# Optimization experiments

Measured on AMD Instinct MI355X. Metric: run time of the kernel, lower is better.

The kernel has to match this reference:

```python
import jax, jax.numpy as jnp
import numpy as np
from jax import lax

L, CB, D, K = 4, 256, 512, 3   # layers, bottleneck, dconv_size, kernel
B, T = 16, 4096                # batch, frames
EPS = 1e-5


def _binarize(w):
    # bitwise weight quantization: sign(w), straight-through in bwd
    return w + lax.stop_gradient(jnp.sign(w) - w)


def _conv1d(x, w, b, dilation=1, groups=1, pad=(0, 0)):
    # x: [N, C, T], w: [O, I/groups, K]
    y = lax.conv_general_dilated(
        x, w, window_strides=(1,), padding=[pad], rhs_dilation=(dilation,),
        dimension_numbers=("NCH", "OIH", "NCH"), feature_group_count=groups)
    return y + b[None, :, None]


def _prelu(x, a):
    return jnp.where(x >= 0, x, a * x)


def _bn(x, g, b):
    # training-mode BatchNorm1d over (batch, time) per channel
    mean = jnp.mean(x, axis=(0, 2), keepdims=True)
    var = jnp.var(x, axis=(0, 2), keepdims=True)
    xn = (x - mean) * lax.rsqrt(var + EPS)
    return xn * g[None, :, None] + b[None, :, None]


def setup_inputs() -> dict:
    key = jax.random.key(0)
    ks = jax.random.split(key, 8)
    s = 0.05
    return {
        "x":   jax.random.normal(ks[0], (B, CB, T), jnp.float32),
        "w1":  jax.random.normal(ks[1], (L, D, CB, 1), jnp.float32) * s,
        "b1":  jnp.zeros((L, D), jnp.float32),
        "a1":  jnp.full((L,), 0.25, jnp.float32),
        "g1":  jnp.ones((L, D), jnp.float32),
        "be1": jnp.zeros((L, D), jnp.float32),
        "wd":  jax.random.normal(ks[2], (L, D, 1, K), jnp.float32) * s,
        "bd":  jnp.zeros((L, D), jnp.float32),
        "a2":  jnp.full((L,), 0.25, jnp.float32),
        "g2":  jnp.ones((L, D), jnp.float32),
        "be2": jnp.zeros((L, D), jnp.float32),
        "w2":  jax.random.normal(ks[3], (L, CB, D, 1), jnp.float32) * s,
        "b2":  jnp.zeros((L, CB), jnp.float32),
    }


def reference(x, w1, b1, a1, g1, be1, wd, bd, a2, g2, be2, w2, b2):
    resid = x
    for i in range(L):
        dil = 2 ** i
        pad_left = dil * (K - 1)  # causal/chomped padding keeps length T
        x = _conv1d(x, _binarize(w1[i]), b1[i])                       # 1x1: CB->D
        x = _bn(_prelu(x, a1[i]), g1[i], be1[i])
        x = _conv1d(x, _binarize(wd[i]), bd[i], dilation=dil,
                    groups=D, pad=(pad_left, 0))                       # depthwise dilated
        x = _bn(_prelu(x, a2[i]), g2[i], be2[i])
        x = _conv1d(x, _binarize(w2[i]), b2[i])                       # 1x1: D->CB
    return x + resid
```

## Files before the change

kernel.cpp:

```cpp
#include <hip/hip_runtime.h>
#include <stdint.h>
#include <stddef.h>

#define NL   4
#define CBC  256
#define DCH  512
#define KW   3
#define BATCH 16
#define TT   4096
#define BT   (BATCH*TT)
#define EPSB 1e-5f

typedef __bf16 bf16_t;
typedef __attribute__((ext_vector_type(8))) __bf16 bf16x8;
typedef __attribute__((ext_vector_type(4))) float f32x4;
typedef __attribute__((ext_vector_type(8))) unsigned short us8;
typedef __attribute__((ext_vector_type(4))) unsigned short us4;

static __device__ __forceinline__ unsigned short f2bf(float f) {
    union { float f; uint32_t u; } v; v.f = f;
    uint32_t u = v.u;
    u += 0x7FFFu + ((u >> 16) & 1u);
    return (unsigned short)(u >> 16);
}
static __device__ __forceinline__ float bf2f(unsigned short b) {
    union { uint32_t u; float f; } v; v.u = ((uint32_t)b) << 16;
    return v.f;
}
static __device__ __forceinline__ bf16x8 as_bf16x8(us8 u) {
    return __builtin_bit_cast(bf16x8, u);
}
static __device__ __forceinline__ float signf_(float w) {
    return (w > 0.f) ? 1.f : ((w < 0.f) ? -1.f : 0.f);
}

typedef __attribute__((address_space(1))) void as1_void;
typedef __attribute__((address_space(3))) void as3_void;
static __device__ __forceinline__ void gload_lds16(const unsigned short* g, unsigned short* l) {
    __builtin_amdgcn_global_load_lds((as1_void*)g, (as3_void*)l, 16, 0, 0);
}

__global__ void prep_kernel(const float* __restrict__ w1, const float* __restrict__ wd,
                            unsigned short* __restrict__ W1S, float* __restrict__ WDS) {
    const int NW1 = NL * DCH * CBC;
    const int NWD = NL * DCH * KW;
    int idx = blockIdx.x * 256 + threadIdx.x;
    if (idx < NW1) {
        W1S[idx] = f2bf(signf_(w1[idx]));
    } else if (idx < NW1 + NWD) {
        int j = idx - NW1;
        WDS[j] = signf_(wd[j]);
    }
}

__global__ void transpose_in(const float* __restrict__ x, unsigned short* __restrict__ XA) {
    __shared__ unsigned short tile[64][72];
    const int t0 = blockIdx.x * 64, c0 = blockIdx.y * 64, b = blockIdx.z;
    const int tid = threadIdx.x;
    {
        const int cl = tid >> 2;
        const int tl = (tid & 3) * 16;
        const float* src = x + ((size_t)(b * CBC + c0 + cl)) * TT + t0 + tl;
        #pragma unroll
        for (int u = 0; u < 16; u += 4) {
            float4 f = *(const float4*)(src + u);
            tile[cl][tl + u + 0] = f2bf(f.x);
            tile[cl][tl + u + 1] = f2bf(f.y);
            tile[cl][tl + u + 2] = f2bf(f.z);
            tile[cl][tl + u + 3] = f2bf(f.w);
        }
    }
    __syncthreads();
    {
        const int tr = tid >> 2;
        const int cc = (tid & 3) * 16;
        us8 o0, o1;
        #pragma unroll
        for (int e = 0; e < 8; ++e) { o0[e] = tile[cc + e][tr]; o1[e] = tile[cc + 8 + e][tr]; }
        unsigned short* dst = XA + ((size_t)(b * TT + t0 + tr)) * CBC + c0 + cc;
        *(us8*)dst = o0;
        *(us8*)(dst + 8) = o1;
    }
}

template<int K, int NMT, bool PRELU, bool FINAL, bool STATS>
__global__ __launch_bounds__(256, 4)
void gemm_kernel(const unsigned short* __restrict__ A,
                 const unsigned short* __restrict__ Bact,
                 const float* __restrict__ bias,
                 const float* __restrict__ aptr,
                 unsigned short* __restrict__ Obf,
                 float* __restrict__ Ofin,
                 const float* __restrict__ resid,
                 float* __restrict__ sums, float* __restrict__ sqs,
                 int M) {
    __shared__ union {
        unsigned short stage[2][4][2048];
        unsigned short sout[128 * 136];
    } sm;
    __shared__ float sstat[2][4][64];

    const int tid = threadIdx.x;

    const int nwg = NMT * (TT / 128) * BATCH;
    const int orig = blockIdx.x;
    const int logical = (orig & 7) * (nwg >> 3) + (orig >> 3);
    const int mt = logical % NMT;
    const int rest = logical / NMT;
    const int tt = rest & 31;
    const int bz = rest >> 5;
    const int t0 = tt * 128;
    const int m0 = mt * 128;
    const size_t n0 = (size_t)bz * TT + t0;

    const int lane = tid & 63;
    const int w    = tid >> 6;
    const int wm = w & 1, wn = w >> 1;
    const int l16 = lane & 15, q = lane >> 4;

    const int rS = tid >> 2;
    const int cS = ((tid & 3) ^ ((tid >> 3) & 3)) * 8;
    const unsigned short* gA0 = A + (size_t)(m0 + rS) * K + cS;
    const unsigned short* gA1 = A + (size_t)(m0 + 64 + rS) * K + cS;
    const unsigned short* gB0 = Bact + (n0 + rS) * K + cS;
    const unsigned short* gB1 = Bact + (n0 + 64 + rS) * K + cS;
    const int wofs = w << 9;

    auto STAGE = [&](int step, int buf) {
        const int k0 = step * 32;
        unsigned short* sb = &sm.stage[buf][0][0];
        gload_lds16(gA0 + k0, sb + 0 * 2048 + wofs);
        gload_lds16(gA1 + k0, sb + 1 * 2048 + wofs);
        gload_lds16(gB0 + k0, sb + 2 * 2048 + wofs);
        gload_lds16(gB1 + k0, sb + 3 * 2048 + wofs);
    };

    f32x4 acc[4][4];
    #pragma unroll
    for (int i = 0; i < 4; ++i)
        #pragma unroll
        for (int j = 0; j < 4; ++j)
            acc[i][j] = (f32x4){0.f, 0.f, 0.f, 0.f};

    const int csw = (q ^ ((l16 >> 1) & 3)) << 3;

    constexpr int NK = K / 32;
    STAGE(0, 0);
    asm volatile("s_waitcnt vmcnt(0)" ::: "memory");
    __builtin_amdgcn_s_barrier();
    __builtin_amdgcn_sched_barrier(0);

    #pragma unroll
    for (int k = 0; k < NK; ++k) {
        const int cur = k & 1;
        if (k + 1 < NK) STAGE(k + 1, cur ^ 1);
        const unsigned short* sb = &sm.stage[cur][0][0];
        bf16x8 af[4], bfv[4];
        #pragma unroll
        for (int i = 0; i < 4; ++i)
            af[i] = as_bf16x8(*(const us8*)(sb + wm * 2048 + (i * 16 + l16) * 32 + csw));
        #pragma unroll
        for (int j = 0; j < 4; ++j)
            bfv[j] = as_bf16x8(*(const us8*)(sb + (2 + wn) * 2048 + (j * 16 + l16) * 32 + csw));
        #pragma unroll
        for (int i = 0; i < 4; ++i)
            #pragma unroll
            for (int j = 0; j < 4; ++j)
                acc[i][j] = __builtin_amdgcn_mfma_f32_16x16x32_bf16(af[i], bfv[j], acc[i][j], 0, 0, 0);
        if (k + 1 < NK) {
            asm volatile("s_waitcnt vmcnt(0)" ::: "memory");
            __builtin_amdgcn_sched_barrier(0);
        }
        __builtin_amdgcn_s_barrier();
        __builtin_amdgcn_sched_barrier(0);
    }

    float alpha = 0.f;
    if constexpr (PRELU) alpha = aptr[0];

    if constexpr (FINAL) {
        #pragma unroll
        for (int i = 0; i < 4; ++i) {
            const int m_l = wm * 64 + i * 16 + q * 4;
            float bia[4];
            #pragma unroll
            for (int rg = 0; rg < 4; ++rg) bia[rg] = bias[m0 + m_l + rg];
            #pragma unroll
            for (int j = 0; j < 4; ++j) {
                const int n_l = wn * 64 + j * 16 + l16;
                const int t = t0 + n_l;
                #pragma unroll
                for (int rg = 0; rg < 4; ++rg) {
                    float v = acc[i][j][rg] + bia[rg];
                    size_t oidx = ((size_t)(bz * CBC + m0 + m_l + rg)) * TT + t;
                    Ofin[oidx] = v + resid[oidx];
                }
            }
        }
    } else {
        #pragma unroll
        for (int i = 0; i < 4; ++i) {
            const int m_l = wm * 64 + i * 16 + q * 4;
            float bia[4];
            #pragma unroll
            for (int rg = 0; rg < 4; ++rg) bia[rg] = bias[m0 + m_l + rg];
            #pragma unroll
            for (int j = 0; j < 4; ++j) {
                const int n_l = wn * 64 + j * 16 + l16;
                us4 pkv;
                #pragma unroll
                for (int rg = 0; rg < 4; ++rg) {
                    float v = acc[i][j][rg] + bia[rg];
                    if (PRELU) v = (v >= 0.f) ? v : alpha * v;
                    pkv[rg] = f2bf(v);
                }
                *(us4*)&sm.sout[n_l * 136 + m_l] = pkv;
            }
            if constexpr (STATS) {
                #pragma unroll
                for (int rg = 0; rg < 4; ++rg) {
                    float sv = 0.f, sq2 = 0.f;
                    #pragma unroll
                    for (int j = 0; j < 4; ++j) {
                        float v = acc[i][j][rg] + bia[rg];
                        if (PRELU) v = (v >= 0.f) ? v : alpha * v;
                        sv += v; sq2 += v * v;
                    }
                    #pragma unroll
                    for (int msk = 1; msk < 16; msk <<= 1) {
                        sv  += __shfl_xor(sv,  msk, 64);
                        sq2 += __shfl_xor(sq2, msk, 64);
                    }
                    if (l16 == 0) {
                        const int cl = i * 16 + q * 4 + rg;
                        sstat[0][w][cl] = sv;
                        sstat[1][w][cl] = sq2;
                    }
                }
            }
        }
        __syncthreads();
        const int rr = tid >> 4;
        const int c8 = (tid & 15) * 8;
        #pragma unroll
        for (int p = 0; p < 8; ++p) {
            const int n_l = p * 16 + rr;
            us8 v = *(const us8*)&sm.sout[n_l * 136 + c8];
            *(us8*)(Obf + (n0 + n_l) * M + m0 + c8) = v;
        }
        if constexpr (STATS) {
            if (tid < 128) {
                const int wmc = tid >> 6, cl = tid & 63;
                float S = sstat[0][wmc][cl] + sstat[0][wmc + 2][cl];
                float Q = sstat[1][wmc][cl] + sstat[1][wmc + 2][cl];
                atomicAdd(&sums[m0 + tid], S);
                atomicAdd(&sqs[m0 + tid], Q);
            }
        }
    }
}

__global__ void bn_finalize(float* __restrict__ sums, float* __restrict__ sqs,
                            const float* __restrict__ g, const float* __restrict__ be,
                            float* __restrict__ scale, float* __restrict__ shift) {
    const int d = threadIdx.x;
    const float inv = 1.f / (float)BT;
    float mean = sums[d] * inv;
    float var = sqs[d] * inv - mean * mean;
    float sc = g[d] * rsqrtf(var + EPSB);
    scale[d] = sc;
    shift[d] = be[d] - mean * sc;
    sums[d] = 0.f;
    sqs[d] = 0.f;
}

__global__ __launch_bounds__(256)
void dwconv_kernel(const unsigned short* __restrict__ Y,
                   const float* __restrict__ scale, const float* __restrict__ shift,
                   const float* __restrict__ wds, const float* __restrict__ bd,
                   const float* __restrict__ a2p, int dil,
                   unsigned short* __restrict__ Z,
                   float* __restrict__ sums, float* __restrict__ sqs) {
    __shared__ float ssum[4][512];
    __shared__ float ssq[4][512];
    const int b = blockIdx.y;
    const int t0 = blockIdx.x * 64;
    const int tid = threadIdx.x;
    const int w = tid >> 6;
    const int lane = tid & 63;
    const int c0 = lane * 8;

    float s[8], sh[8], w0[8], w1[8], w2[8], bb[8];
    #pragma unroll
    for (int e = 0; e < 8; ++e) {
        int d = c0 + e;
        s[e] = scale[d]; sh[e] = shift[d];
        w0[e] = wds[d * 3 + 0]; w1[e] = wds[d * 3 + 1]; w2[e] = wds[d * 3 + 2];
        bb[e] = bd[d];
    }
    const float alpha = a2p[0];
    float asum[8], asq[8];
    #pragma unroll
    for (int e = 0; e < 8; ++e) { asum[e] = 0.f; asq[e] = 0.f; }

    for (int it = 0; it < 16; ++it) {
        const int t = t0 + it * 4 + w;
        const size_t base = ((size_t)b * TT + t) * DCH + c0;
        float acc[8];
        {
            us8 y0 = *(const us8*)&Y[base];
            #pragma unroll
            for (int e = 0; e < 8; ++e)
                acc[e] = w2[e] * (s[e] * bf2f(y0[e]) + sh[e]) + bb[e];
        }
        if (t >= dil) {
            us8 y1 = *(const us8*)&Y[base - (size_t)dil * DCH];
            #pragma unroll
            for (int e = 0; e < 8; ++e)
                acc[e] += w1[e] * (s[e] * bf2f(y1[e]) + sh[e]);
        }
        if (t >= 2 * dil) {
            us8 y2 = *(const us8*)&Y[base - (size_t)(2 * dil) * DCH];
            #pragma unroll
            for (int e = 0; e < 8; ++e)
                acc[e] += w0[e] * (s[e] * bf2f(y2[e]) + sh[e]);
        }
        us8 o;
        #pragma unroll
        for (int e = 0; e < 8; ++e) {
            float v = acc[e];
            v = (v >= 0.f) ? v : alpha * v;
            asum[e] += v; asq[e] += v * v;
            o[e] = f2bf(v);
        }
        *(us8*)&Z[base] = o;
    }

    #pragma unroll
    for (int e = 0; e < 8; ++e) { ssum[w][c0 + e] = asum[e]; ssq[w][c0 + e] = asq[e]; }
    __syncthreads();
    {
        const int ch0 = tid * 2;
        #pragma unroll
        for (int u = 0; u < 2; ++u) {
            const int ch = ch0 + u;
            float S = ssum[0][ch] + ssum[1][ch] + ssum[2][ch] + ssum[3][ch];
            float Q = ssq[0][ch] + ssq[1][ch] + ssq[2][ch] + ssq[3][ch];
            atomicAdd(&sums[ch], S);
            atomicAdd(&sqs[ch], Q);
        }
    }
}

__global__ void fold_kernel(const float* __restrict__ w2,
                            const float* __restrict__ scale2, const float* __restrict__ shift2,
                            const float* __restrict__ b2,
                            unsigned short* __restrict__ W2E, float* __restrict__ B2E) {
    __shared__ float red[256];
    const int c = blockIdx.x, tid = threadIdx.x;
    float part = 0.f;
    for (int d = tid; d < DCH; d += 256) {
        float w = w2[(size_t)c * DCH + d];
        float sgn = signf_(w);
        W2E[(size_t)c * DCH + d] = f2bf(sgn * scale2[d]);
        part += sgn * shift2[d];
    }
    red[tid] = part;
    __syncthreads();
    for (int off = 128; off > 0; off >>= 1) {
        if (tid < off) red[tid] += red[tid + off];
        __syncthreads();
    }
    if (tid == 0) B2E[c] = b2[c] + red[0];
}

extern "C" void kernel_launch(void* const* d_in, const int* in_sizes, int n_in,
                              void* d_out, int out_size, void* d_ws, size_t ws_size,
                              hipStream_t stream) {
    const float* x   = (const float*)d_in[0];
    const float* w1  = (const float*)d_in[1];
    const float* b1  = (const float*)d_in[2];
    const float* a1  = (const float*)d_in[3];
    const float* g1  = (const float*)d_in[4];
    const float* be1 = (const float*)d_in[5];
    const float* wd  = (const float*)d_in[6];
    const float* bd  = (const float*)d_in[7];
    const float* a2  = (const float*)d_in[8];
    const float* g2  = (const float*)d_in[9];
    const float* be2 = (const float*)d_in[10];
    const float* w2  = (const float*)d_in[11];
    const float* b2  = (const float*)d_in[12];
    float* out = (float*)d_out;

    char* ws = (char*)d_ws;
    size_t off = 0;
    auto alloc = [&](size_t bytes) -> void* {
        void* p = ws + off;
        off += (bytes + 255) & ~(size_t)255;
        return p;
    };
    unsigned short* XA  = (unsigned short*)alloc((size_t)BT * CBC * 2);
    unsigned short* Y   = (unsigned short*)alloc((size_t)BT * DCH * 2);
    unsigned short* Z   = (unsigned short*)alloc((size_t)BT * DCH * 2);
    unsigned short* W1S = (unsigned short*)alloc((size_t)NL * DCH * CBC * 2);
    float* WDS          = (float*)alloc((size_t)NL * DCH * KW * 4);
    unsigned short* W2E = (unsigned short*)alloc((size_t)CBC * DCH * 2);
    float* B2E          = (float*)alloc((size_t)CBC * 4);
    float* sums   = (float*)alloc(512 * 4);
    float* sqs    = (float*)alloc(512 * 4);
    float* scale1 = (float*)alloc(512 * 4);
    float* shift1 = (float*)alloc(512 * 4);
    float* scale2 = (float*)alloc(512 * 4);
    float* shift2 = (float*)alloc(512 * 4);

    (void)hipMemsetAsync(sums, 0, 512 * 4, stream);
    (void)hipMemsetAsync(sqs, 0, 512 * 4, stream);

    {
        const int NTOT = NL * DCH * CBC + NL * DCH * KW;
        prep_kernel<<<(NTOT + 255) / 256, 256, 0, stream>>>(w1, wd, W1S, WDS);
    }
    transpose_in<<<dim3(TT / 64, CBC / 64, BATCH), 256, 0, stream>>>(x, XA);

    const int NWG1 = (DCH / 128) * (TT / 128) * BATCH;
    const int NWG2 = (CBC / 128) * (TT / 128) * BATCH;

    for (int l = 0; l < NL; ++l) {
        gemm_kernel<CBC, DCH / 128, true, false, true><<<NWG1, 256, 0, stream>>>(
            W1S + (size_t)l * DCH * CBC, XA, b1 + (size_t)l * DCH, a1 + l,
            Y, nullptr, nullptr, sums, sqs, DCH);
        bn_finalize<<<1, 512, 0, stream>>>(sums, sqs, g1 + (size_t)l * DCH, be1 + (size_t)l * DCH,
                                           scale1, shift1);
        dwconv_kernel<<<dim3(TT / 64, BATCH), 256, 0, stream>>>(
            Y, scale1, shift1, WDS + (size_t)l * DCH * KW, bd + (size_t)l * DCH, a2 + l, 1 << l,
            Z, sums, sqs);
        bn_finalize<<<1, 512, 0, stream>>>(sums, sqs, g2 + (size_t)l * DCH, be2 + (size_t)l * DCH,
                                           scale2, shift2);
        fold_kernel<<<CBC, 256, 0, stream>>>(w2 + (size_t)l * CBC * DCH, scale2, shift2,
                                             b2 + (size_t)l * CBC, W2E, B2E);
        if (l < NL - 1) {
            gemm_kernel<DCH, CBC / 128, false, false, false><<<NWG2, 256, 0, stream>>>(
                W2E, Z, B2E, nullptr, XA, nullptr, nullptr, nullptr, nullptr, CBC);
        } else {
            gemm_kernel<DCH, CBC / 128, false, true, false><<<NWG2, 256, 0, stream>>>(
                W2E, Z, B2E, nullptr, nullptr, out, x, nullptr, nullptr, CBC);
        }
    }
}
```

Measured before the change: 721.3 us.

## Fold BN finalize into consumers and restructure depthwise conv with prefetch

Removes both bn_finalize launches by computing scale and shift from the raw sums inside dwconv and fold, using per-layer stat buffers that are zeroed once up front. The depthwise conv halves its time tile (more blocks), sets a launch-bounds occupancy hint, and for interior tiles folds the BN scale and shift into the conv weights with software-prefetched loads. Each thread now recomputes the BN parameters redundantly, and the shift folding assumes all three taps are in range, which the boundary block path handles separately.

After: 945.1 us. 31.0% more time.

```diff
diff --git a/kernel.cpp b/kernel.cpp
--- a/kernel.cpp
+++ b/kernel.cpp
@@ -10,6 +10,7 @@
 #define TT   4096
 #define BT   (BATCH*TT)
 #define EPSB 1e-5f
+#define DWT  32
 
 typedef __bf16 bf16_t;
 typedef __attribute__((ext_vector_type(8))) __bf16 bf16x8;
@@ -260,80 +261,113 @@
     }
 }
 
-__global__ void bn_finalize(float* __restrict__ sums, float* __restrict__ sqs,
-                            const float* __restrict__ g, const float* __restrict__ be,
-                            float* __restrict__ scale, float* __restrict__ shift) {
-    const int d = threadIdx.x;
-    const float inv = 1.f / (float)BT;
-    float mean = sums[d] * inv;
-    float var = sqs[d] * inv - mean * mean;
-    float sc = g[d] * rsqrtf(var + EPSB);
-    scale[d] = sc;
-    shift[d] = be[d] - mean * sc;
-    sums[d] = 0.f;
-    sqs[d] = 0.f;
-}
-
-__global__ __launch_bounds__(256)
+__global__ __launch_bounds__(256, 4)
 void dwconv_kernel(const unsigned short* __restrict__ Y,
-                   const float* __restrict__ scale, const float* __restrict__ shift,
+                   const float* __restrict__ sums1, const float* __restrict__ sqs1,
+                   const float* __restrict__ g1, const float* __restrict__ be1,
                    const float* __restrict__ wds, const float* __restrict__ bd,
                    const float* __restrict__ a2p, int dil,
                    unsigned short* __restrict__ Z,
-                   float* __restrict__ sums, float* __restrict__ sqs) {
+                   float* __restrict__ sums2, float* __restrict__ sqs2) {
     __shared__ float ssum[4][512];
     __shared__ float ssq[4][512];
     const int b = blockIdx.y;
-    const int t0 = blockIdx.x * 64;
+    const int t0 = blockIdx.x * DWT;
     const int tid = threadIdx.x;
     const int w = tid >> 6;
     const int lane = tid & 63;
     const int c0 = lane * 8;
-
-    float s[8], sh[8], w0[8], w1[8], w2[8], bb[8];
+    const float alpha = a2p[0];
+    constexpr int NIT = DWT / 4;
+
+    float s8[8], sh8[8], wv0[8], wv1[8], wv2[8], bb8[8];
+    const float inv = 1.f / (float)BT;
     #pragma unroll
     for (int e = 0; e < 8; ++e) {
-        int d = c0 + e;
-        s[e] = scale[d]; sh[e] = shift[d];
-        w0[e] = wds[d * 3 + 0]; w1[e] = wds[d * 3 + 1]; w2[e] = wds[d * 3 + 2];
-        bb[e] = bd[d];
-    }
-    const float alpha = a2p[0];
+        const int d = c0 + e;
+        float mean = sums1[d] * inv;
+        float var = sqs1[d] * inv - mean * mean;
+        float sc = g1[d] * rsqrtf(var + EPSB);
+        s8[e] = sc;
+        sh8[e] = be1[d] - mean * sc;
+        wv0[e] = wds[d * 3 + 0]; wv1[e] = wds[d * 3 + 1]; wv2[e] = wds[d * 3 + 2];
+        bb8[e] = bd[d];
+    }
+
     float asum[8], asq[8];
     #pragma unroll
     for (int e = 0; e < 8; ++e) { asum[e] = 0.f; asq[e] = 0.f; }
 
-    for (int it = 0; it < 16; ++it) {
-        const int t = t0 + it * 4 + w;
-        const size_t base = ((size_t)b * TT + t) * DCH + c0;
-        float acc[8];
-        {
-            us8 y0 = *(const us8*)&Y[base];
-            #pragma unroll
-            for (int e = 0; e < 8; ++e)
-                acc[e] = w2[e] * (s[e] * bf2f(y0[e]) + sh[e]) + bb[e];
-        }
-        if (t >= dil) {
-            us8 y1 = *(const us8*)&Y[base - (size_t)dil * DCH];
-            #pragma unroll
-            for (int e = 0; e < 8; ++e)
-                acc[e] += w1[e] * (s[e] * bf2f(y1[e]) + sh[e]);
-        }
-        if (t >= 2 * dil) {
-            us8 y2 = *(const us8*)&Y[base - (size_t)(2 * dil) * DCH];
-            #pragma unroll
-            for (int e = 0; e < 8; ++e)
-                acc[e] += w0[e] * (s[e] * bf2f(y2[e]) + sh[e]);
-        }
-        us8 o;
+    if (blockIdx.x == 0) {
+        for (int it = 0; it < NIT; ++it) {
+            const int t = t0 + it * 4 + w;
+            const size_t base = ((size_t)b * TT + t) * DCH + c0;
+            float acc[8];
+            {
+                us8 y0 = *(const us8*)&Y[base];
+                #pragma unroll
+                for (int e = 0; e < 8; ++e)
+                    acc[e] = wv2[e] * (s8[e] * bf2f(y0[e]) + sh8[e]) + bb8[e];
+            }
+            if (t >= dil) {
+                us8 y1 = *(const us8*)&Y[base - (size_t)dil * DCH];
+                #pragma unroll
+                for (int e = 0; e < 8; ++e)
+                    acc[e] += wv1[e] * (s8[e] * bf2f(y1[e]) + sh8[e]);
+            }
+            if (t >= 2 * dil) {
+                us8 y2 = *(const us8*)&Y[base - (size_t)(2 * dil) * DCH];
+                #pragma unroll
+                for (int e = 0; e < 8; ++e)
+                    acc[e] += wv0[e] * (s8[e] * bf2f(y2[e]) + sh8[e]);
+            }
+            us8 o;
+            #pragma unroll
+            for (int e = 0; e < 8; ++e) {
+                float v = acc[e];
+                v = (v >= 0.f) ? v : alpha * v;
+                asum[e] += v; asq[e] += v * v;
+                o[e] = f2bf(v);
+            }
+            *(us8*)&Z[base] = o;
+        }
+    } else {
+        float W0s[8], W1s[8], W2s[8], shall[8];
         #pragma unroll
         for (int e = 0; e < 8; ++e) {
-            float v = acc[e];
-            v = (v >= 0.f) ? v : alpha * v;
-            asum[e] += v; asq[e] += v * v;
-            o[e] = f2bf(v);
-        }
-        *(us8*)&Z[base] = o;
+            W0s[e] = wv0[e] * s8[e];
+            W1s[e] = wv1[e] * s8[e];
+            W2s[e] = wv2[e] * s8[e];
+            shall[e] = (wv0[e] + wv1[e] + wv2[e]) * sh8[e] + bb8[e];
+        }
+        const size_t base0 = ((size_t)b * TT + t0 + w) * DCH + c0;
+        const size_t dstep = (size_t)4 * DCH;
+        const size_t d1 = (size_t)dil * DCH, d2 = 2 * d1;
+
+        us8 y0c = *(const us8*)&Y[base0];
+        us8 y1c = *(const us8*)&Y[base0 - d1];
+        us8 y2c = *(const us8*)&Y[base0 - d2];
+        #pragma unroll
+        for (int it = 0; it < NIT; ++it) {
+            us8 y0n, y1n, y2n;
+            if (it + 1 < NIT) {
+                const size_t bn = base0 + (size_t)(it + 1) * dstep;
+                y0n = *(const us8*)&Y[bn];
+                y1n = *(const us8*)&Y[bn - d1];
+                y2n = *(const us8*)&Y[bn - d2];
+            }
+            us8 o;
+            #pragma unroll
+            for (int e = 0; e < 8; ++e) {
+                float v = W2s[e] * bf2f(y0c[e]) + W1s[e] * bf2f(y1c[e])
+                        + W0s[e] * bf2f(y2c[e]) + shall[e];
+                v = (v >= 0.f) ? v : alpha * v;
+                asum[e] += v; asq[e] += v * v;
+                o[e] = f2bf(v);
+            }
+            *(us8*)&Z[base0 + (size_t)it * dstep] = o;
+            y0c = y0n; y1c = y1n; y2c = y2n;
+        }
     }
 
     #pragma unroll
@@ -346,24 +380,30 @@
             const int ch = ch0 + u;
             float S = ssum[0][ch] + ssum[1][ch] + ssum[2][ch] + ssum[3][ch];
             float Q = ssq[0][ch] + ssq[1][ch] + ssq[2][ch] + ssq[3][ch];
-            atomicAdd(&sums[ch], S);
-            atomicAdd(&sqs[ch], Q);
+            atomicAdd(&sums2[ch], S);
+            atomicAdd(&sqs2[ch], Q);
         }
     }
 }
 
 __global__ void fold_kernel(const float* __restrict__ w2,
-                            const float* __restrict__ scale2, const float* __restrict__ shift2,
+                            const float* __restrict__ sums2, const float* __restrict__ sqs2,
+                            const float* __restrict__ g2, const float* __restrict__ be2,
                             const float* __restrict__ b2,
                             unsigned short* __restrict__ W2E, float* __restrict__ B2E) {
     __shared__ float red[256];
     const int c = blockIdx.x, tid = threadIdx.x;
+    const float inv = 1.f / (float)BT;
     float part = 0.f;
     for (int d = tid; d < DCH; d += 256) {
+        float mean = sums2[d] * inv;
+        float var = sqs2[d] * inv - mean * mean;
+        float sc = g2[d] * rsqrtf(var + EPSB);
+        float shf = be2[d] - mean * sc;
         float w = w2[(size_t)c * DCH + d];
         float sgn = signf_(w);
-        W2E[(size_t)c * DCH + d] = f2bf(sgn * scale2[d]);
-        part += sgn * shift2[d];
+        W2E[(size_t)c * DCH + d] = f2bf(sgn * sc);
+        part += sgn * shf;
     }
     red[tid] = part;
     __syncthreads();
@@ -406,15 +446,13 @@
     float* WDS          = (float*)alloc((size_t)NL * DCH * KW * 4);
     unsigned short* W2E = (unsigned short*)alloc((size_t)CBC * DCH * 2);
     float* B2E          = (float*)alloc((size_t)CBC * 4);
-    float* sums   = (float*)alloc(512 * 4);
-    float* sqs    = (float*)alloc(512 * 4);
-    float* scale1 = (float*)alloc(512 * 4);
-    float* shift1 = (float*)alloc(512 * 4);
-    float* scale2 = (float*)alloc(512 * 4);
-    float* shift2 = (float*)alloc(512 * 4);
-
-    (void)hipMemsetAsync(sums, 0, 512 * 4, stream);
-    (void)hipMemsetAsync(sqs, 0, 512 * 4, stream);
+    float* stats = (float*)alloc((size_t)4 * NL * 512 * 4);
+    float* sums1 = stats + 0 * NL * 512;
+    float* sqs1  = stats + 1 * NL * 512;
+    float* sums2 = stats + 2 * NL * 512;
+    float* sqs2  = stats + 3 * NL * 512;
+
+    (void)hipMemsetAsync(stats, 0, (size_t)4 * NL * 512 * 4, stream);
 
     {
         const int NTOT = NL * DCH * CBC + NL * DCH * KW;
@@ -428,15 +466,14 @@
     for (int l = 0; l < NL; ++l) {
         gemm_kernel<CBC, DCH / 128, true, false, true><<<NWG1, 256, 0, stream>>>(
             W1S + (size_t)l * DCH * CBC, XA, b1 + (size_t)l * DCH, a1 + l,
-            Y, nullptr, nullptr, sums, sqs, DCH);
-        bn_finalize<<<1, 512, 0, stream>>>(sums, sqs, g1 + (size_t)l * DCH, be1 + (size_t)l * DCH,
-                                           scale1, shift1);
-        dwconv_kernel<<<dim3(TT / 64, BATCH), 256, 0, stream>>>(
-            Y, scale1, shift1, WDS + (size_t)l * DCH * KW, bd + (size_t)l * DCH, a2 + l, 1 << l,
-            Z, sums, sqs);
-        bn_finalize<<<1, 512, 0, stream>>>(sums, sqs, g2 + (size_t)l * DCH, be2 + (size_t)l * DCH,
-                                           scale2, shift2);
-        fold_kernel<<<CBC, 256, 0, stream>>>(w2 + (size_t)l * CBC * DCH, scale2, shift2,
+            Y, nullptr, nullptr, sums1 + l * 512, sqs1 + l * 512, DCH);
+        dwconv_kernel<<<dim3(TT / DWT, BATCH), 256, 0, stream>>>(
+            Y, sums1 + l * 512, sqs1 + l * 512, g1 + (size_t)l * DCH, be1 + (size_t)l * DCH,
+            WDS + (size_t)l * DCH * KW, bd + (size_t)l * DCH, a2 + l, 1 << l,
+            Z, sums2 + l * 512, sqs2 + l * 512);
+        fold_kernel<<<CBC, 256, 0, stream>>>(w2 + (size_t)l * CBC * DCH,
+                                             sums2 + l * 512, sqs2 + l * 512,
+                                             g2 + (size_t)l * DCH, be2 + (size_t)l * DCH,
                                              b2 + (size_t)l * CBC, W2E, B2E);
         if (l < NL - 1) {
             gemm_kernel<DCH, CBC / 128, false, false, false><<<NWG2, 256, 0, stream>>>(
```
